# Optimization experiments

Measured on AMD Instinct MI355X. Metric: run time of the kernel, lower is better.

## Reference

```python
import jax, jax.numpy as jnp
import numpy as np

BETA = 0.9
THRESH = 1.0
ALPHA = 2.0  # snntorch ATan surrogate default

@jax.custom_vjp
def atan_spike(x):
    return (x > 0).astype(x.dtype)

def _atan_fwd(x):
    return atan_spike(x), x

def _atan_bwd(x, g):
    # d/dx of snntorch ATan surrogate: (alpha/2) / (1 + (pi/2*alpha*x)^2)
    return (g * (ALPHA / 2) / (1 + (jnp.pi / 2 * ALPHA * x) ** 2),)

atan_spike.defvjp(_atan_fwd, _atan_bwd)

def setup_inputs() -> dict:
    key = jax.random.key(0)
    k1, k2, k3, k4, k5 = jax.random.split(key, 5)
    B, T, F, H, O = 256, 1024, 64, 512, 64
    x = jax.random.normal(k1, (B, T, F), dtype=jnp.float32)
    s_in = 1.0 / np.sqrt(F)
    s_out = 1.0 / np.sqrt(H)
    W_in = jax.random.uniform(k2, (H, F), jnp.float32, -s_in, s_in)
    b_in = jax.random.uniform(k3, (H,), jnp.float32, -s_in, s_in)
    W_out = jax.random.uniform(k4, (O, H), jnp.float32, -s_out, s_out)
    b_out = jax.random.uniform(k5, (O,), jnp.float32, -s_out, s_out)
    return {"x": x, "W_in": W_in, "b_in": b_in, "W_out": W_out, "b_out": b_out}

def reference(x, W_in, b_in, W_out, b_out):
    B, T, F = x.shape
    H = W_in.shape[0]
    O = W_out.shape[0]
    dt = x.dtype
    # precompute input currents for all steps: [T, B, H]
    cur1_all = jnp.einsum('btf,hf->tbh', x, W_in) + b_in

    def step(carry, cur1):
        mem1, mem_out = carry
        # snntorch Leaky(subtract): reset from previous mem (detached),
        # then mem = beta*mem + input - reset*threshold, spike from new mem.
        reset1 = jax.lax.stop_gradient((mem1 > THRESH).astype(dt))
        mem1 = BETA * mem1 + cur1 - reset1 * THRESH
        spk1 = atan_spike(mem1 - THRESH)
        cur_out = spk1 @ W_out.T + b_out
        reset_o = jax.lax.stop_gradient((mem_out > THRESH).astype(dt))
        mem_out = BETA * mem_out + cur_out - reset_o * THRESH
        spk_out = atan_spike(mem_out - THRESH)
        return (mem1, mem_out), (mem_out, spk_out)

    init = (jnp.zeros((B, H), dt), jnp.zeros((B, O), dt))
    _, (mem_rec, spk_rec) = jax.lax.scan(step, init, cur1_all)
    # [T, B, O] -> [B, T, O]
    return mem_rec.transpose(1, 0, 2), spk_rec.transpose(1, 0, 2)
```

## Files before the change

kernel.cpp:

```cpp
#include <hip/hip_runtime.h>


namespace {
constexpr int kB = 256;
constexpr int kT = 1024;
constexpr int kF = 64;
constexpr int kH = 512;
constexpr int kO = 64;
constexpr float kBeta = 0.9f;
constexpr float kThresh = 1.0f;
constexpr int kThreads = 512;
}

__global__ __launch_bounds__(256)
void warm_x_kernel(const float4* __restrict__ p, int n4) {
  float acc = 0.0f;
  for (int i = blockIdx.x * blockDim.x + threadIdx.x; i < n4;
       i += gridDim.x * blockDim.x) {
    const float4 v = p[i];
    acc += v.x + v.y + v.z + v.w;
  }
  asm volatile("" ::"v"(acc));
}

__global__ __launch_bounds__(kThreads)
__attribute__((amdgpu_waves_per_eu(2, 2)))
void snn_fused5(const float* __restrict__ x,
                const float* __restrict__ W_in,
                const float* __restrict__ b_in,
                const float* __restrict__ W_out,
                const float* __restrict__ b_out,
                float* __restrict__ out) {
  const int b = blockIdx.x;
  const int j = threadIdx.x;
  const int o = j & 63;
  const int s = j >> 6;

  __shared__ float red[2][8][64];

  float win[kF];
  {
    const float4* wiv = reinterpret_cast<const float4*>(W_in) + j * 16;
#pragma unroll
    for (int q = 0; q < 16; ++q) {
      const float4 v = wiv[q];
      win[4 * q + 0] = v.x; win[4 * q + 1] = v.y;
      win[4 * q + 2] = v.z; win[4 * q + 3] = v.w;
    }
  }
  float wout[64];
  {
    const float4* wov =
        reinterpret_cast<const float4*>(W_out) + o * 128 + s * 16;
#pragma unroll
    for (int q = 0; q < 16; ++q) {
      const float4 v = wov[q];
      wout[4 * q + 0] = v.x; wout[4 * q + 1] = v.y;
      wout[4 * q + 2] = v.z; wout[4 * q + 3] = v.w;
    }
  }
  float bin_j = b_in[j];
  float bout_o = b_out[o];

#define PIN8(p)                                                            \
  asm volatile("" : "+v"((p)[0]), "+v"((p)[1]), "+v"((p)[2]),              \
                    "+v"((p)[3]), "+v"((p)[4]), "+v"((p)[5]),              \
                    "+v"((p)[6]), "+v"((p)[7]))
  PIN8(win + 0);  PIN8(win + 8);  PIN8(win + 16); PIN8(win + 24);
  PIN8(win + 32); PIN8(win + 40); PIN8(win + 48); PIN8(win + 56);
  PIN8(wout + 0);  PIN8(wout + 8);  PIN8(wout + 16); PIN8(wout + 24);
  PIN8(wout + 32); PIN8(wout + 40); PIN8(wout + 48); PIN8(wout + 56);
#undef PIN8
  asm volatile("" : "+v"(bin_j), "+v"(bout_o));

  float mem1 = 0.0f, rst1 = 0.0f;
  float memo = 0.0f, rsto = 0.0f;
  unsigned long long mask = 0ull;

  const float4* xv = reinterpret_cast<const float4*>(x + (size_t)b * kT * kF);
  float* out_mem = out + (size_t)b * kT * kO + o;
  float* out_spk = out_mem + (size_t)kB * kT * kO;

  float4 x0, x1, x2, x3, x4, x5, x6, x7, x8, x9, x10, x11, x12, x13, x14, x15;

#define LOADX(tt)                                                          \
  do {                                                                     \
    const float4* xp = xv + (size_t)(tt) * 16;                             \
    x0 = xp[0]; x1 = xp[1]; x2 = xp[2]; x3 = xp[3];                        \
    x4 = xp[4]; x5 = xp[5]; x6 = xp[6]; x7 = xp[7];                        \
    x8 = xp[8]; x9 = xp[9]; x10 = xp[10]; x11 = xp[11];                    \
    x12 = xp[12]; x13 = xp[13]; x14 = xp[14]; x15 = xp[15];                \
  } while (0)

#define BARRIER() asm volatile("s_waitcnt lgkmcnt(0)\n\ts_barrier" ::: "memory")

#define L1Q(q)                                                             \
  c0 = fmaf(x##q.x, win[4 * q + 0], c0);                                   \
  c1 = fmaf(x##q.y, win[4 * q + 1], c1);                                   \
  c2 = fmaf(x##q.z, win[4 * q + 2], c2);                                   \
  c3 = fmaf(x##q.w, win[4 * q + 3], c3);

#define LAYER1()                                                           \
  do {                                                                     \
    float c0 = bin_j, c1 = 0.0f, c2 = 0.0f, c3 = 0.0f;                     \
    L1Q(0) L1Q(1) L1Q(2) L1Q(3) L1Q(4) L1Q(5) L1Q(6) L1Q(7)                \
    L1Q(8) L1Q(9) L1Q(10) L1Q(11) L1Q(12) L1Q(13) L1Q(14) L1Q(15)          \
    const float cur1 = (c0 + c1) + (c2 + c3);                              \
    mem1 = kBeta * mem1 + cur1 - rst1;                                     \
    const bool p = mem1 > kThresh;                                         \
    mask = __ballot(p);                                                    \
    rst1 = p ? 1.0f : 0.0f;                                                \
  } while (0)

#define L2QS(q)                                                            \
  {                                                                        \
    const float f0 = ((mlo >> (4 * (q) + 0)) & 1u) ? 1.0f : 0.0f;          \
    const float f1 = ((mlo >> (4 * (q) + 1)) & 1u) ? 1.0f : 0.0f;          \
    const float f2 = ((mlo >> (4 * (q) + 2)) & 1u) ? 1.0f : 0.0f;          \
    const float f3 = ((mlo >> (4 * (q) + 3)) & 1u) ? 1.0f : 0.0f;          \
    a0 = fmaf(f0, wout[4 * (q) + 0], a0);                                  \
    a1 = fmaf(f1, wout[4 * (q) + 1], a1);                                  \
    a2 = fmaf(f2, wout[4 * (q) + 2], a2);                                  \
    a3 = fmaf(f3, wout[4 * (q) + 3], a3);                                  \
  }

#define L2E(acc, q, i)                                                     \
  acc = acc + __uint_as_float(                                             \
      (unsigned)__builtin_amdgcn_sbfe((int)vmhi, 4 * (q) + (i)-32, 1) &    \
      __float_as_uint(wout[4 * (q) + (i)]));
#define L2QV(q)                                                            \
  { L2E(a0, q, 0) L2E(a1, q, 1) L2E(a2, q, 2) L2E(a3, q, 3) }

#define LAYER2(buf)                                                        \
  do {                                                                     \
    const unsigned mlo = (unsigned)mask;                                   \
    unsigned vmhi = (unsigned)(mask >> 32);                                \
    asm volatile("" : "+v"(vmhi));      \
    float a0 = 0.0f, a1 = 0.0f, a2 = 0.0f, a3 = 0.0f;                      \
    L2QS(0) L2QS(1) L2QS(2) L2QS(3) L2QS(4) L2QS(5) L2QS(6) L2QS(7)        \
    L2QV(8) L2QV(9) L2QV(10) L2QV(11) L2QV(12) L2QV(13) L2QV(14) L2QV(15)  \
    red[(buf)][s][o] = (a0 + a1) + (a2 + a3);                              \
  } while (0)

  LOADX(0);
  LAYER1();
  LOADX(1);

  for (int t = 1; t < kT; ++t) {
    LAYER2((t - 1) & 1);
    BARRIER();

    float r0, r1, r2, r3, r4, r5, r6, r7;
    const int buf = (t - 1) & 1;
    if (s == 0) {
      r0 = red[buf][0][o]; r1 = red[buf][1][o];
      r2 = red[buf][2][o]; r3 = red[buf][3][o];
      r4 = red[buf][4][o]; r5 = red[buf][5][o];
      r6 = red[buf][6][o]; r7 = red[buf][7][o];
    }

    LAYER1();
    const int tn = (t + 1 < kT) ? (t + 1) : (kT - 1);
    LOADX(tn);

    if (s == 0) {
      float co = bout_o;
      co += r0; co += r1; co += r2; co += r3;
      co += r4; co += r5; co += r6; co += r7;
      memo = kBeta * memo + co - rsto;
      const float so = (memo > kThresh) ? 1.0f : 0.0f;
      rsto = so;
      out_mem[(t - 1) * kO] = memo;
      out_spk[(t - 1) * kO] = so;
    }
  }

  LAYER2((kT - 1) & 1);
  BARRIER();
  if (s == 0) {
    const int buf = (kT - 1) & 1;
    float co = bout_o;
    co += red[buf][0][o]; co += red[buf][1][o];
    co += red[buf][2][o]; co += red[buf][3][o];
    co += red[buf][4][o]; co += red[buf][5][o];
    co += red[buf][6][o]; co += red[buf][7][o];
    memo = kBeta * memo + co - rsto;
    const float so = (memo > kThresh) ? 1.0f : 0.0f;
    out_mem[(kT - 1) * kO] = memo;
    out_spk[(kT - 1) * kO] = so;
  }

#undef LOADX
#undef BARRIER
#undef L1Q
#undef LAYER1
#undef L2QS
#undef L2E
#undef L2QV
#undef LAYER2
}

extern "C" void kernel_launch(void* const* d_in, const int* in_sizes, int n_in,
                              void* d_out, int out_size, void* d_ws,
                              size_t ws_size, hipStream_t stream) {
  const float* x = (const float*)d_in[0];
  const float* W_in = (const float*)d_in[1];
  const float* b_in = (const float*)d_in[2];
  const float* W_out = (const float*)d_in[3];
  const float* b_out = (const float*)d_in[4];
  float* out = (float*)d_out;

  const int n4 = kB * kT * kF / 4;
  hipLaunchKernelGGL(warm_x_kernel, dim3(1024), dim3(256), 0, stream,
                     (const float4*)x, n4);
  hipLaunchKernelGGL(snn_fused5, dim3(kB), dim3(kThreads), 0, stream,
                     x, W_in, b_in, W_out, b_out, out);
}
```

Baseline: 1.101 ms.

## Split input projection into chunked parallel kernel feeding a lighter recurrent kernel

The layer-1 input projection moves out of the serial recurrence into a separate fully parallel kernel. It writes cur1 for a time chunk into workspace, and a recurrent kernel then consumes it, carrying state across chunks through global memory. Layer 2 now reads spikes with readlane broadcasts instead of ballot bit extraction. This takes 64 FMAs per step off the serial critical path, at the cost of extra global traffic for cur1, extra kernel launches, and state save and restore between chunks. If the workspace is too small, the old fused kernel runs instead.

```diff
diff --git a/kernel.cpp b/kernel.cpp
--- a/kernel.cpp
+++ b/kernel.cpp
@@ -9,8 +9,188 @@
 constexpr int kO = 64;
 constexpr float kBeta = 0.9f;
 constexpr float kThresh = 1.0f;
-constexpr int kThreads = 512;
-}
+}
+
+#define PIN8(p)                                                            \
+  asm volatile("" : "+v"((p)[0]), "+v"((p)[1]), "+v"((p)[2]),              \
+                    "+v"((p)[3]), "+v"((p)[4]), "+v"((p)[5]),              \
+                    "+v"((p)[6]), "+v"((p)[7]))
+
+#define FMA4(v, q)                                                         \
+  c0 = fmaf((v).x, win[4 * (q) + 0], c0);                                  \
+  c1 = fmaf((v).y, win[4 * (q) + 1], c1);                                  \
+  c2 = fmaf((v).z, win[4 * (q) + 2], c2);                                  \
+  c3 = fmaf((v).w, win[4 * (q) + 3], c3);
+
+__global__ __launch_bounds__(512, 4)
+void snn_cur1(const float* __restrict__ x, const float* __restrict__ W_in,
+              const float* __restrict__ b_in, float* __restrict__ cur1,
+              int t0, int ntc) {
+  const int lane = threadIdx.x & 63;
+  const int s = threadIdx.x >> 6;
+  const int h = s * 64 + lane;
+  const int bpb = ntc >> 7;
+  const int b = blockIdx.x / bpb;
+  const int tcbase = (blockIdx.x - b * bpb) * 128;
+
+  float win[kF];
+  {
+    const float4* wiv = reinterpret_cast<const float4*>(W_in) + h * 16;
+#pragma unroll
+    for (int q = 0; q < 16; ++q) {
+      const float4 v = wiv[q];
+      win[4 * q + 0] = v.x; win[4 * q + 1] = v.y;
+      win[4 * q + 2] = v.z; win[4 * q + 3] = v.w;
+    }
+  }
+  float bin_h = b_in[h];
+  PIN8(win + 0);  PIN8(win + 8);  PIN8(win + 16); PIN8(win + 24);
+  PIN8(win + 32); PIN8(win + 40); PIN8(win + 48); PIN8(win + 56);
+  asm volatile("" : "+v"(bin_h));
+
+  const float* xbase = x + ((size_t)b * kT + t0 + tcbase) * kF;
+  float* cbase = cur1 + ((size_t)b * ntc + tcbase) * (size_t)kH + h;
+
+  for (int i = 0; i < 128; ++i) {
+    const float4* xp = reinterpret_cast<const float4*>(xbase + (size_t)i * kF);
+    float4 xa0 = xp[0], xa1 = xp[1], xa2 = xp[2], xa3 = xp[3];
+    float4 xb0 = xp[4], xb1 = xp[5], xb2 = xp[6], xb3 = xp[7];
+    float c0 = bin_h, c1 = 0.0f, c2 = 0.0f, c3 = 0.0f;
+    FMA4(xa0, 0) FMA4(xa1, 1) FMA4(xa2, 2) FMA4(xa3, 3)
+    xa0 = xp[8]; xa1 = xp[9]; xa2 = xp[10]; xa3 = xp[11];
+    FMA4(xb0, 4) FMA4(xb1, 5) FMA4(xb2, 6) FMA4(xb3, 7)
+    xb0 = xp[12]; xb1 = xp[13]; xb2 = xp[14]; xb3 = xp[15];
+    FMA4(xa0, 8) FMA4(xa1, 9) FMA4(xa2, 10) FMA4(xa3, 11)
+    FMA4(xb0, 12) FMA4(xb1, 13) FMA4(xb2, 14) FMA4(xb3, 15)
+    cbase[(size_t)i * kH] = (c0 + c1) + (c2 + c3);
+  }
+}
+
+#define SPK(k)                                                             \
+  __int_as_float(__builtin_amdgcn_readlane(__float_as_int(rst1), (k)))
+
+#define L2RL(q)                                                            \
+  a0 = fmaf(SPK(4 * (q) + 0), wout[4 * (q) + 0], a0);                      \
+  a1 = fmaf(SPK(4 * (q) + 1), wout[4 * (q) + 1], a1);                      \
+  a2 = fmaf(SPK(4 * (q) + 2), wout[4 * (q) + 2], a2);                      \
+  a3 = fmaf(SPK(4 * (q) + 3), wout[4 * (q) + 3], a3);
+
+#define LAYER2(buf)                                                        \
+  do {                                                                     \
+    float a0 = 0.0f, a1 = 0.0f, a2 = 0.0f, a3 = 0.0f;                      \
+    L2RL(0) L2RL(1) L2RL(2) L2RL(3) L2RL(4) L2RL(5) L2RL(6) L2RL(7)        \
+    L2RL(8) L2RL(9) L2RL(10) L2RL(11) L2RL(12) L2RL(13) L2RL(14) L2RL(15)  \
+    red[(buf)][s][o] = (a0 + a1) + (a2 + a3);                              \
+  } while (0)
+
+#define BARRIER() asm volatile("s_waitcnt lgkmcnt(0)\n\ts_barrier" ::: "memory")
+
+#define CONSUME(tt)                                                        \
+  do {                                                                     \
+    float co = bout_o;                                                     \
+    co += rr0; co += rr1; co += rr2; co += rr3;                            \
+    co += rr4; co += rr5; co += rr6; co += rr7;                            \
+    memo = kBeta * memo + co - rsto;                                       \
+    const float so = (memo > kThresh) ? 1.0f : 0.0f;                       \
+    rsto = so;                                                             \
+    om[(size_t)(tt) * kO] = memo;                                          \
+    os[(size_t)(tt) * kO] = so;                                            \
+  } while (0)
+
+#define ISSUE_RR(buf)                                                      \
+  do {                                                                     \
+    rr0 = red[buf][0][o]; rr1 = red[buf][1][o];                            \
+    rr2 = red[buf][2][o]; rr3 = red[buf][3][o];                            \
+    rr4 = red[buf][4][o]; rr5 = red[buf][5][o];                            \
+    rr6 = red[buf][6][o]; rr7 = red[buf][7][o];                            \
+  } while (0)
+
+#define L1STEP(PF)                                                         \
+  do {                                                                     \
+    mem1 = kBeta * mem1 + (PF)-rst1;                                       \
+    const bool p = mem1 > kThresh;                                         \
+    rst1 = p ? 1.0f : 0.0f;                                                \
+  } while (0)
+
+__global__ __launch_bounds__(512, 2)
+void snn_rec(const float* __restrict__ cur1, const float* __restrict__ W_out,
+             const float* __restrict__ b_out, float* __restrict__ out,
+             float* __restrict__ state, int t0, int ntc) {
+  const int b = blockIdx.x;
+  const int j = threadIdx.x;
+  const int o = j & 63;
+  const int s = j >> 6;
+
+  __shared__ float red[2][8][64];
+
+  float wout[kO];
+  {
+    const float4* wov =
+        reinterpret_cast<const float4*>(W_out) + o * (kH / 4) + s * 16;
+#pragma unroll
+    for (int q = 0; q < 16; ++q) {
+      const float4 v = wov[q];
+      wout[4 * q + 0] = v.x; wout[4 * q + 1] = v.y;
+      wout[4 * q + 2] = v.z; wout[4 * q + 3] = v.w;
+    }
+  }
+  float bout_o = b_out[o];
+  PIN8(wout + 0);  PIN8(wout + 8);  PIN8(wout + 16); PIN8(wout + 24);
+  PIN8(wout + 32); PIN8(wout + 40); PIN8(wout + 48); PIN8(wout + 56);
+  asm volatile("" : "+v"(bout_o));
+
+  float* m1s = state;
+  float* r1s = state + kB * kH;
+  float* mos = state + 2 * kB * kH;
+  float* ros = mos + kB * kO;
+  const int idx1 = b * kH + j;
+  const int idxo = b * kO + o;
+
+  float mem1 = 0.0f, rst1 = 0.0f, memo = 0.0f, rsto = 0.0f;
+  if (t0 != 0) {
+    mem1 = m1s[idx1];
+    rst1 = r1s[idx1];
+    if (s == 0) { memo = mos[idxo]; rsto = ros[idxo]; }
+  }
+
+  const float* cp = cur1 + (size_t)b * ntc * kH + j;
+  float* om = out + ((size_t)b * kT + t0) * kO + o;
+  float* os = om + (size_t)kB * kT * kO;
+
+  float rr0, rr1, rr2, rr3, rr4, rr5, rr6, rr7;
+  float pfa = cp[0];
+  float pfb = cp[(size_t)1 * kH];
+
+  for (int tc = 0; tc < ntc; tc += 2) {
+    L1STEP(pfa);
+    {
+      const int tp = (tc + 2 < ntc) ? tc + 2 : ntc - 1;
+      pfa = cp[(size_t)tp * kH];
+    }
+    LAYER2(0);
+    if (s == 0 && tc != 0) CONSUME(tc - 1);
+    BARRIER();
+    if (s == 0) ISSUE_RR(0);
+
+    L1STEP(pfb);
+    {
+      const int tp = (tc + 3 < ntc) ? tc + 3 : ntc - 1;
+      pfb = cp[(size_t)tp * kH];
+    }
+    LAYER2(1);
+    if (s == 0) CONSUME(tc);
+    BARRIER();
+    if (s == 0) ISSUE_RR(1);
+  }
+  if (s == 0) CONSUME(ntc - 1);
+
+  m1s[idx1] = mem1;
+  r1s[idx1] = rst1;
+  if (s == 0) { mos[idxo] = memo; ros[idxo] = rsto; }
+}
+
+#define BITF(k) ((((k) < 32 ? (mlo >> (k)) : (mhi >> ((k)-32))) & 1u) \
+                 ? 1.0f : 0.0f)
 
 __global__ __launch_bounds__(256)
 void warm_x_kernel(const float4* __restrict__ p, int n4) {
@@ -23,28 +203,24 @@
   asm volatile("" ::"v"(acc));
 }
 
-__global__ __launch_bounds__(kThreads)
+__global__ __launch_bounds__(512)
 __attribute__((amdgpu_waves_per_eu(2, 2)))
-void snn_fused5(const float* __restrict__ x,
-                const float* __restrict__ W_in,
+void snn_fused5(const float* __restrict__ x, const float* __restrict__ W_in,
                 const float* __restrict__ b_in,
                 const float* __restrict__ W_out,
-                const float* __restrict__ b_out,
-                float* __restrict__ out) {
+                const float* __restrict__ b_out, float* __restrict__ out) {
   const int b = blockIdx.x;
   const int j = threadIdx.x;
   const int o = j & 63;
   const int s = j >> 6;
-
   __shared__ float red[2][8][64];
-
   float win[kF];
   {
     const float4* wiv = reinterpret_cast<const float4*>(W_in) + j * 16;
 #pragma unroll
     for (int q = 0; q < 16; ++q) {
       const float4 v = wiv[q];
-      win[4 * q + 0] = v.x; win[4 * q + 1] = v.y;
+      win[4 * q] = v.x; win[4 * q + 1] = v.y;
       win[4 * q + 2] = v.z; win[4 * q + 3] = v.w;
     }
   }
@@ -55,34 +231,23 @@
 #pragma unroll
     for (int q = 0; q < 16; ++q) {
       const float4 v = wov[q];
-      wout[4 * q + 0] = v.x; wout[4 * q + 1] = v.y;
+      wout[4 * q] = v.x; wout[4 * q + 1] = v.y;
       wout[4 * q + 2] = v.z; wout[4 * q + 3] = v.w;
     }
   }
   float bin_j = b_in[j];
   float bout_o = b_out[o];
-
-#define PIN8(p)                                                            \
-  asm volatile("" : "+v"((p)[0]), "+v"((p)[1]), "+v"((p)[2]),              \
-                    "+v"((p)[3]), "+v"((p)[4]), "+v"((p)[5]),              \
-                    "+v"((p)[6]), "+v"((p)[7]))
   PIN8(win + 0);  PIN8(win + 8);  PIN8(win + 16); PIN8(win + 24);
   PIN8(win + 32); PIN8(win + 40); PIN8(win + 48); PIN8(win + 56);
   PIN8(wout + 0);  PIN8(wout + 8);  PIN8(wout + 16); PIN8(wout + 24);
   PIN8(wout + 32); PIN8(wout + 40); PIN8(wout + 48); PIN8(wout + 56);
-#undef PIN8
   asm volatile("" : "+v"(bin_j), "+v"(bout_o));
-
-  float mem1 = 0.0f, rst1 = 0.0f;
-  float memo = 0.0f, rsto = 0.0f;
+  float mem1 = 0.0f, rst1 = 0.0f, memo = 0.0f, rsto = 0.0f;
   unsigned long long mask = 0ull;
-
   const float4* xv = reinterpret_cast<const float4*>(x + (size_t)b * kT * kF);
   float* out_mem = out + (size_t)b * kT * kO + o;
   float* out_spk = out_mem + (size_t)kB * kT * kO;
-
   float4 x0, x1, x2, x3, x4, x5, x6, x7, x8, x9, x10, x11, x12, x13, x14, x15;
-
 #define LOADX(tt)                                                          \
   do {                                                                     \
     const float4* xp = xv + (size_t)(tt) * 16;                             \
@@ -91,16 +256,12 @@
     x8 = xp[8]; x9 = xp[9]; x10 = xp[10]; x11 = xp[11];                    \
     x12 = xp[12]; x13 = xp[13]; x14 = xp[14]; x15 = xp[15];                \
   } while (0)
-
-#define BARRIER() asm volatile("s_waitcnt lgkmcnt(0)\n\ts_barrier" ::: "memory")
-
 #define L1Q(q)                                                             \
   c0 = fmaf(x##q.x, win[4 * q + 0], c0);                                   \
   c1 = fmaf(x##q.y, win[4 * q + 1], c1);                                   \
   c2 = fmaf(x##q.z, win[4 * q + 2], c2);                                   \
   c3 = fmaf(x##q.w, win[4 * q + 3], c3);
-
-#define LAYER1()                                                           \
+#define LAYER1F()                                                          \
   do {                                                                     \
     float c0 = bin_j, c1 = 0.0f, c2 = 0.0f, c3 = 0.0f;                     \
     L1Q(0) L1Q(1) L1Q(2) L1Q(3) L1Q(4) L1Q(5) L1Q(6) L1Q(7)                \
@@ -111,7 +272,6 @@
     mask = __ballot(p);                                                    \
     rst1 = p ? 1.0f : 0.0f;                                                \
   } while (0)
-
 #define L2QS(q)                                                            \
   {                                                                        \
     const float f0 = ((mlo >> (4 * (q) + 0)) & 1u) ? 1.0f : 0.0f;          \
@@ -123,33 +283,28 @@
     a2 = fmaf(f2, wout[4 * (q) + 2], a2);                                  \
     a3 = fmaf(f3, wout[4 * (q) + 3], a3);                                  \
   }
-
 #define L2E(acc, q, i)                                                     \
   acc = acc + __uint_as_float(                                             \
       (unsigned)__builtin_amdgcn_sbfe((int)vmhi, 4 * (q) + (i)-32, 1) &    \
       __float_as_uint(wout[4 * (q) + (i)]));
 #define L2QV(q)                                                            \
   { L2E(a0, q, 0) L2E(a1, q, 1) L2E(a2, q, 2) L2E(a3, q, 3) }
-
-#define LAYER2(buf)                                                        \
+#define LAYER2F(buf)                                                       \
   do {                                                                     \
     const unsigned mlo = (unsigned)mask;                                   \
     unsigned vmhi = (unsigned)(mask >> 32);                                \
-    asm volatile("" : "+v"(vmhi));      \
+    asm volatile("" : "+v"(vmhi));                                         \
     float a0 = 0.0f, a1 = 0.0f, a2 = 0.0f, a3 = 0.0f;                      \
     L2QS(0) L2QS(1) L2QS(2) L2QS(3) L2QS(4) L2QS(5) L2QS(6) L2QS(7)        \
     L2QV(8) L2QV(9) L2QV(10) L2QV(11) L2QV(12) L2QV(13) L2QV(14) L2QV(15)  \
     red[(buf)][s][o] = (a0 + a1) + (a2 + a3);                              \
   } while (0)
-
   LOADX(0);
-  LAYER1();
+  LAYER1F();
   LOADX(1);
-
   for (int t = 1; t < kT; ++t) {
-    LAYER2((t - 1) & 1);
+    LAYER2F((t - 1) & 1);
     BARRIER();
-
     float r0, r1, r2, r3, r4, r5, r6, r7;
     const int buf = (t - 1) & 1;
     if (s == 0) {
@@ -158,11 +313,9 @@
       r4 = red[buf][4][o]; r5 = red[buf][5][o];
       r6 = red[buf][6][o]; r7 = red[buf][7][o];
     }
-
-    LAYER1();
+    LAYER1F();
     const int tn = (t + 1 < kT) ? (t + 1) : (kT - 1);
     LOADX(tn);
-
     if (s == 0) {
       float co = bout_o;
       co += r0; co += r1; co += r2; co += r3;
@@ -174,8 +327,7 @@
       out_spk[(t - 1) * kO] = so;
     }
   }
-
-  LAYER2((kT - 1) & 1);
+  LAYER2F((kT - 1) & 1);
   BARRIER();
   if (s == 0) {
     const int buf = (kT - 1) & 1;
@@ -189,15 +341,6 @@
     out_mem[(kT - 1) * kO] = memo;
     out_spk[(kT - 1) * kO] = so;
   }
-
-#undef LOADX
-#undef BARRIER
-#undef L1Q
-#undef LAYER1
-#undef L2QS
-#undef L2E
-#undef L2QV
-#undef LAYER2
 }
 
 extern "C" void kernel_launch(void* const* d_in, const int* in_sizes, int n_in,
@@ -210,9 +353,29 @@
   const float* b_out = (const float*)d_in[4];
   float* out = (float*)d_out;
 
-  const int n4 = kB * kT * kF / 4;
-  hipLaunchKernelGGL(warm_x_kernel, dim3(1024), dim3(256), 0, stream,
-                     (const float4*)x, n4);
-  hipLaunchKernelGGL(snn_fused5, dim3(kB), dim3(kThreads), 0, stream,
-                     x, W_in, b_in, W_out, b_out, out);
-}
+  const size_t state_bytes = ((size_t)2 * kB * kH + 2 * kB * kO) * 4;
+  int nch = 0;
+  for (int c : {4, 8}) {
+    const size_t need = (size_t)kB * (kT / c) * kH * 4 + state_bytes;
+    if (need <= ws_size) { nch = c; break; }
+  }
+
+  if (nch) {
+    const int ntc = kT / nch;
+    float* cur1 = (float*)d_ws;
+    float* state = cur1 + (size_t)kB * ntc * kH;
+    const int g1 = kB * (ntc / 128);
+    for (int c = 0; c < nch; ++c) {
+      hipLaunchKernelGGL(snn_cur1, dim3(g1), dim3(512), 0, stream,
+                         x, W_in, b_in, cur1, c * ntc, ntc);
+      hipLaunchKernelGGL(snn_rec, dim3(kB), dim3(512), 0, stream,
+                         cur1, W_out, b_out, out, state, c * ntc, ntc);
+    }
+  } else {
+    const int n4 = kB * kT * kF / 4;
+    hipLaunchKernelGGL(warm_x_kernel, dim3(1024), dim3(256), 0, stream,
+                       (const float4*)x, n4);
+    hipLaunchKernelGGL(snn_fused5, dim3(kB), dim3(512), 0, stream,
+                       x, W_in, b_in, W_out, b_out, out);
+  }
+}
```

New measurement: 1.560 ms. 41.6% more time.
